# Optimization experiments

Hardware: AMD Instinct MI355X
Metric: run time of the kernel (lower is better)

Reference implementation:

```python
import jax, jax.numpy as jnp
import numpy as np

LN_EPS = 1e-3   # keras LayerNormalization default epsilon
STAB = 1e-3     # performer relu-kernel numerical stabilizer
N = 2           # number of blocks per branch


def layer_norm(x, g, b):
    m = jnp.mean(x, axis=-1, keepdims=True)
    v = jnp.mean(jnp.square(x - m), axis=-1, keepdims=True)
    return (x - m) * jax.lax.rsqrt(v + LN_EPS) * g + b


def favor(q_in, kv_in, Wq, Wk, Wv, Wo):
    # Performer FAVOR attention, relu kernel features (google-research fast_attention,
    # projection_matrix_type=None). q/k/v head projections have no bias.
    q = jnp.einsum('bld,dhm->blhm', q_in, Wq)
    k = jnp.einsum('bsd,dhm->bshm', kv_in, Wk)
    v = jnp.einsum('bsd,dhm->bshm', kv_in, Wv)
    norm = q.shape[-1] ** -0.25  # 1/sqrt(sqrt(head_dim))
    qp = jax.nn.relu(q * norm) + STAB
    kp = jax.nn.relu(k * norm) + STAB
    kv = jnp.einsum('bshm,bshd->bhmd', kp, v)
    num = jnp.einsum('blhm,bhmd->blhd', qp, kv)
    den = jnp.einsum('blhm,bhm->blh', qp, kp.sum(axis=1))
    out = num / den[..., None]
    return jnp.einsum('blhd,hde->ble', out, Wo)


def forward(obj_inputs, road_inputs,
            rg_dense_W, rg_dense_b, rg_qkv_W, rg_qkv_b,
            rg_Wq, rg_Wk, rg_Wv, rg_Wo, rg_ln_g, rg_ln_b, rg_fc_W, rg_fc_b,
            rg_out_W, rg_out_b,
            dense_W, dense_b, pos_emb,
            Wq, Wk, Wv, Wo, ln_g, ln_b, fc_W, fc_b):
    rgH = rg_dense_W.shape[1]
    # ---- roadgraph branch: performer self-attention blocks ----
    x = jax.nn.relu(road_inputs @ rg_dense_W + rg_dense_b)
    for i in range(N):
        qkv = jax.nn.relu(x @ rg_qkv_W + rg_qkv_b)
        q = qkv[..., :rgH]  # k,v splits unused by FastSelfAttention (it re-projects q)
        attn = favor(q, q, rg_Wq[i], rg_Wk[i], rg_Wv[i], rg_Wo[i])
        n = layer_norm(attn + x, rg_ln_g[i], rg_ln_b[i])
        y = jax.nn.relu(n @ rg_fc_W[i] + rg_fc_b[i])
        x = layer_norm(n + y, rg_ln_g[i], rg_ln_b[i])  # original reuses ln_block_1
    rg_out = jax.nn.relu(x @ rg_out_W + rg_out_b)
    # ---- object branch: performer cross-attention blocks ----
    x = jax.nn.relu(obj_inputs @ dense_W + dense_b)
    x = x + pos_emb  # learned position embedding, [T, H]
    for i in range(N):
        attn = favor(x, rg_out, Wq[i], Wk[i], Wv[i], Wo[i])
        n = layer_norm(attn + x, ln_g[i], ln_b[i])
        y = jax.nn.relu(n @ fc_W[i] + fc_b[i])
        x = layer_norm(n + y, ln_g[i], ln_b[i])  # original reuses ln_block_1
    return x


def setup_inputs() -> dict:
    B, T, V = 8, 128, 512
    S, F = 8192, 8
    rgH, H = 16, 1024
    rh, rd = 4, 4     # rg heads, head_dim
    h, d = 16, 64     # cross heads, head_dim
    keys = iter(jax.random.split(jax.random.key(0), 64))
    def rnd(shape, scale=1.0):
        return jax.random.normal(next(keys), shape, dtype=jnp.float32) * scale
    return {
        'obj_inputs': rnd((B, T, V)),
        'road_inputs': rnd((B, S, F)),
        'rg_dense_W': rnd((F, rgH), F ** -0.5), 'rg_dense_b': jnp.zeros((rgH,), jnp.float32),
        'rg_qkv_W': rnd((rgH, 3 * rgH), rgH ** -0.5), 'rg_qkv_b': jnp.zeros((3 * rgH,), jnp.float32),
        'rg_Wq': rnd((N, rgH, rh, rd), rgH ** -0.5),
        'rg_Wk': rnd((N, rgH, rh, rd), rgH ** -0.5),
        'rg_Wv': rnd((N, rgH, rh, rd), rgH ** -0.5),
        'rg_Wo': rnd((N, rh, rd, rgH), rgH ** -0.5),
        'rg_ln_g': jnp.ones((N, rgH), jnp.float32), 'rg_ln_b': jnp.zeros((N, rgH), jnp.float32),
        'rg_fc_W': rnd((N, rgH, rgH), rgH ** -0.5), 'rg_fc_b': jnp.zeros((N, rgH), jnp.float32),
        'rg_out_W': rnd((rgH, H), rgH ** -0.5), 'rg_out_b': jnp.zeros((H,), jnp.float32),
        'dense_W': rnd((V, H), V ** -0.5), 'dense_b': jnp.zeros((H,), jnp.float32),
        'pos_emb': rnd((T, H), 0.02),
        'Wq': rnd((N, H, h, d), H ** -0.5),
        'Wk': rnd((N, H, h, d), H ** -0.5),
        'Wv': rnd((N, H, h, d), H ** -0.5),
        'Wo': rnd((N, h, d, H), H ** -0.5),
        'ln_g': jnp.ones((N, H), jnp.float32), 'ln_b': jnp.zeros((N, H), jnp.float32),
        'fc_W': rnd((N, H, H), H ** -0.5), 'fc_b': jnp.zeros((N, H), jnp.float32),
    }


def reference(obj_inputs, road_inputs, rg_dense_W, rg_dense_b, rg_qkv_W, rg_qkv_b,
              rg_Wq, rg_Wk, rg_Wv, rg_Wo, rg_ln_g, rg_ln_b, rg_fc_W, rg_fc_b,
              rg_out_W, rg_out_b, dense_W, dense_b, pos_emb,
              Wq, Wk, Wv, Wo, ln_g, ln_b, fc_W, fc_b):
    return forward(obj_inputs, road_inputs, rg_dense_W, rg_dense_b, rg_qkv_W, rg_qkv_b,
                   rg_Wq, rg_Wk, rg_Wv, rg_Wo, rg_ln_g, rg_ln_b, rg_fc_W, rg_fc_b,
                   rg_out_W, rg_out_b, dense_W, dense_b, pos_emb,
                   Wq, Wk, Wv, Wo, ln_g, ln_b, fc_W, fc_b)
```

## Files before the change

kernel.cpp:

```cpp
#include <hip/hip_runtime.h>

typedef unsigned short u16;
typedef unsigned int u32;

using s8v = __attribute__((ext_vector_type(8))) short;
using f4v = __attribute__((ext_vector_type(4))) float;

#define LN_EPS 0.001f
#define STAB 0.001f
#define NORM_OBJ 0.35355339059327373f
#define NORM_ROAD 0.7071067811865476f

__device__ __forceinline__ float bf2f(u16 v) { return __uint_as_float(((u32)v) << 16); }
__device__ __forceinline__ u16 f2bf(float f) {
  u32 u = __float_as_uint(f);
  u32 r = (u + 0x7fffu + ((u >> 16) & 1u)) >> 16;
  return (u16)r;
}
__device__ __forceinline__ f4v mfma16(s8v a, s8v b, f4v c) {
  return __builtin_amdgcn_mfma_f32_16x16x32_bf16(a, b, c, 0, 0, 0);
}
__device__ __forceinline__ void ldsload16(void* lds, const void* g) {
  __builtin_amdgcn_global_load_lds((const __attribute__((address_space(1))) u32*)g,
                                   (__attribute__((address_space(3))) u32*)lds, 16, 0, 0);
}

struct TPair { const float* s; u16* d; };
struct TP11 { TPair p[11]; };

__global__ __launch_bounds__(256) void transpose_kernel(TP11 ps, int K, int N) {
  const float* __restrict__ src = ps.p[blockIdx.z].s;
  u16* __restrict__ dst = ps.p[blockIdx.z].d;
  int n0 = blockIdx.x * 64, k0 = blockIdx.y * 64;
  int t = threadIdx.x;
  __shared__ __align__(16) u16 lt[64 * 72];
#pragma unroll
  for (int j = 0; j < 4; ++j) {
    int p = t + 256 * j;
    int r = p >> 4, cb = p & 15;
    float4 v = *(const float4*)(src + (size_t)(k0 + r) * N + n0 + cb * 4);
    lt[r * 72 + cb * 4 + 0] = f2bf(v.x);
    lt[r * 72 + cb * 4 + 1] = f2bf(v.y);
    lt[r * 72 + cb * 4 + 2] = f2bf(v.z);
    lt[r * 72 + cb * 4 + 3] = f2bf(v.w);
  }
  __syncthreads();
#pragma unroll
  for (int j = 0; j < 2; ++j) {
    int q = t + 256 * j;
    int on = q >> 3, ocb = q & 7;
    u16 e[8];
#pragma unroll
    for (int i = 0; i < 8; ++i) e[i] = lt[(ocb * 8 + i) * 72 + on];
    uint4 v;
    v.x = (u32)e[0] | ((u32)e[1] << 16);
    v.y = (u32)e[2] | ((u32)e[3] << 16);
    v.z = (u32)e[4] | ((u32)e[5] << 16);
    v.w = (u32)e[6] | ((u32)e[7] << 16);
    *(uint4*)(dst + (size_t)(n0 + on) * K + k0 + ocb * 8) = v;
  }
}

__global__ __launch_bounds__(256) void cvt_kernel(const float* __restrict__ src,
                                                  u16* __restrict__ dst) {
  int i = (blockIdx.x * 256 + threadIdx.x) * 4;
  float4 v = *(const float4*)(src + i);
  uint2 o;
  o.x = (u32)f2bf(v.x) | ((u32)f2bf(v.y) << 16);
  o.y = (u32)f2bf(v.z) | ((u32)f2bf(v.w) << 16);
  *(uint2*)(dst + i) = o;
}

__global__ __launch_bounds__(256) void r0_kernel(const float* __restrict__ road,
    const float* __restrict__ W, const float* __restrict__ bias, float* __restrict__ x) {
  int row = blockIdx.x * 256 + threadIdx.x;
  float in[8];
  float4 v0 = *(const float4*)(road + (size_t)row * 8);
  float4 v1 = *(const float4*)(road + (size_t)row * 8 + 4);
  in[0] = v0.x; in[1] = v0.y; in[2] = v0.z; in[3] = v0.w;
  in[4] = v1.x; in[5] = v1.y; in[6] = v1.z; in[7] = v1.w;
#pragma unroll
  for (int j = 0; j < 16; ++j) {
    float s = bias[j];
#pragma unroll
    for (int c = 0; c < 8; ++c) s += in[c] * W[c * 16 + j];
    x[(size_t)row * 16 + j] = fmaxf(s, 0.f);
  }
}

__global__ __launch_bounds__(256) void ra_kernel(const float* __restrict__ x,
    const float* __restrict__ qkvW, const float* __restrict__ qkvb,
    const float* __restrict__ Wk, const float* __restrict__ Wv,
    float* __restrict__ kvr, float* __restrict__ ksr) {
  int t = threadIdx.x;
  int row = blockIdx.x * 256 + t;
  int b = row >> 13;
  float xv[16];
#pragma unroll
  for (int e = 0; e < 16; ++e) xv[e] = x[(size_t)row * 16 + e];
  float q16[16];
#pragma unroll
  for (int j = 0; j < 16; ++j) {
    float s = qkvb[j];
#pragma unroll
    for (int c = 0; c < 16; ++c) s += xv[c] * qkvW[c * 48 + j];
    q16[j] = fmaxf(s, 0.f);
  }
  float kp[16], vh[16];
#pragma unroll
  for (int hm = 0; hm < 16; ++hm) {
    float sk = 0.f, sv = 0.f;
#pragma unroll
    for (int c = 0; c < 16; ++c) {
      float q = q16[c];
      sk += q * Wk[c * 16 + hm];
      sv += q * Wv[c * 16 + hm];
    }
    kp[hm] = fmaxf(sk * NORM_ROAD, 0.f) + STAB;
    vh[hm] = sv;
  }
  __shared__ float l[80];
  if (t < 80) l[t] = 0.f;
  __syncthreads();
#pragma unroll
  for (int h = 0; h < 4; ++h)
#pragma unroll
    for (int m = 0; m < 4; ++m) {
      float kpv = kp[h * 4 + m];
      atomicAdd(&l[64 + h * 4 + m], kpv);
#pragma unroll
      for (int d = 0; d < 4; ++d) atomicAdd(&l[h * 16 + m * 4 + d], kpv * vh[h * 4 + d]);
    }
  __syncthreads();
  if (t < 64) atomicAdd(&kvr[b * 64 + t], l[t]);
  else if (t < 80) atomicAdd(&ksr[b * 16 + (t - 64)], l[t]);
}

__device__ __forceinline__ void ln16(const float* tv, const float* g, const float* bb, float* o) {
  float m = 0.f;
#pragma unroll
  for (int e = 0; e < 16; ++e) m += tv[e];
  m *= (1.f / 16.f);
  float var = 0.f;
#pragma unroll
  for (int e = 0; e < 16; ++e) { float d = tv[e] - m; var += d * d; }
  var *= (1.f / 16.f);
  float rstd = rsqrtf(var + LN_EPS);
#pragma unroll
  for (int e = 0; e < 16; ++e) o[e] = (tv[e] - m) * rstd * g[e] + bb[e];
}

__global__ __launch_bounds__(256) void rb_kernel(float* __restrict__ x,
    const float* __restrict__ qkvW, const float* __restrict__ qkvb,
    const float* __restrict__ Wq, const float* __restrict__ Wo,
    const float* __restrict__ lng, const float* __restrict__ lnb,
    const float* __restrict__ fcW, const float* __restrict__ fcb,
    const float* __restrict__ kvr, const float* __restrict__ ksr) {
  int row = blockIdx.x * 256 + threadIdx.x;
  int b = row >> 13;
  float xv[16];
#pragma unroll
  for (int e = 0; e < 16; ++e) xv[e] = x[(size_t)row * 16 + e];
  float q16[16];
#pragma unroll
  for (int j = 0; j < 16; ++j) {
    float s = qkvb[j];
#pragma unroll
    for (int c = 0; c < 16; ++c) s += xv[c] * qkvW[c * 48 + j];
    q16[j] = fmaxf(s, 0.f);
  }
  float qp[16];
#pragma unroll
  for (int hm = 0; hm < 16; ++hm) {
    float s = 0.f;
#pragma unroll
    for (int c = 0; c < 16; ++c) s += q16[c] * Wq[c * 16 + hm];
    qp[hm] = fmaxf(s * NORM_ROAD, 0.f) + STAB;
  }
  float attn[16];
#pragma unroll
  for (int e = 0; e < 16; ++e) attn[e] = 0.f;
#pragma unroll
  for (int h = 0; h < 4; ++h) {
    float den = 0.f;
#pragma unroll
    for (int m = 0; m < 4; ++m) den += qp[h * 4 + m] * ksr[b * 16 + h * 4 + m];
    float od[4];
#pragma unroll
    for (int d = 0; d < 4; ++d) {
      float num = 0.f;
#pragma unroll
      for (int m = 0; m < 4; ++m) num += qp[h * 4 + m] * kvr[b * 64 + h * 16 + m * 4 + d];
      od[d] = num / den;
    }
#pragma unroll
    for (int d = 0; d < 4; ++d)
#pragma unroll
      for (int e = 0; e < 16; ++e) attn[e] += od[d] * Wo[(h * 4 + d) * 16 + e];
  }
  float tv[16], n[16], o2[16];
#pragma unroll
  for (int e = 0; e < 16; ++e) tv[e] = attn[e] + xv[e];
  ln16(tv, lng, lnb, n);
#pragma unroll
  for (int j = 0; j < 16; ++j) {
    float s = fcb[j];
#pragma unroll
    for (int e = 0; e < 16; ++e) s += n[e] * fcW[e * 16 + j];
    tv[j] = n[j] + fmaxf(s, 0.f);
  }
  ln16(tv, lng, lnb, o2);
#pragma unroll
  for (int e = 0; e < 16; ++e) x[(size_t)row * 16 + e] = o2[e];
}

__global__ __launch_bounds__(256) void rc_kernel(const float* __restrict__ x,
    const float* __restrict__ W, const float* __restrict__ bias, u16* __restrict__ out) {
  const int t = threadIdx.x;
  const int cg = t & 63, rg = t >> 6;
  const int c0 = blockIdx.x * 256 + cg * 4;
  const int r0 = blockIdx.y * 16;
  __shared__ float lx[256];
  lx[t] = x[(size_t)(r0 + (t >> 4)) * 16 + (t & 15)];
  __syncthreads();
  float4 wv[16];
#pragma unroll
  for (int c = 0; c < 16; ++c) wv[c] = *(const float4*)(W + (size_t)c * 1024 + c0);
  float4 bv = *(const float4*)(bias + c0);
#pragma unroll
  for (int k = 0; k < 4; ++k) {
    int rr = rg * 4 + k;
    float s0 = bv.x, s1 = bv.y, s2 = bv.z, s3 = bv.w;
#pragma unroll
    for (int c = 0; c < 16; ++c) {
      float xv = lx[rr * 16 + c];
      s0 += xv * wv[c].x; s1 += xv * wv[c].y; s2 += xv * wv[c].z; s3 += xv * wv[c].w;
    }
    uint2 o;
    o.x = (u32)f2bf(fmaxf(s0, 0.f)) | ((u32)f2bf(fmaxf(s1, 0.f)) << 16);
    o.y = (u32)f2bf(fmaxf(s2, 0.f)) | ((u32)f2bf(fmaxf(s3, 0.f)) << 16);
    *(uint2*)(out + (size_t)(r0 + rr) * 1024 + c0) = o;
  }
}

__global__ __launch_bounds__(256) void gemm_kernel(
    const u16* __restrict__ A, const u16* __restrict__ BT, int K,
    float* __restrict__ outF, u16* __restrict__ outB,
    const float* __restrict__ bias, const float* __restrict__ resF, int resmod,
    float scale, int do_relu, float post) {
  const int n0 = blockIdx.x * 128, m0 = blockIdx.y * 128;
  const int t = threadIdx.x;
  const int wid = t >> 6, lane = t & 63, quad = lane >> 4, m16 = lane & 15;
  const int wm = wid >> 1, wn = wid & 1;
  const int lrr = lane >> 3;
  const int lcs = (((lane & 7) ^ lrr) * 8);
  const int sw = m16 & 7;
  __shared__ __align__(16) u16 smem[2 * 128 * 64];
  u16* Al = smem;
  u16* Bl = smem + 128 * 64;
  f4v acc[4][4];
#pragma unroll
  for (int i = 0; i < 4; ++i)
#pragma unroll
    for (int j = 0; j < 4; ++j) acc[i][j] = {0.f, 0.f, 0.f, 0.f};

  for (int kc = 0; kc < K; kc += 64) {
    __syncthreads();
#pragma unroll
    for (int j = 0; j < 4; ++j) {
      int rbase = wid * 32 + j * 8;
      ldsload16(Al + rbase * 64, A + (size_t)(m0 + rbase + lrr) * K + kc + lcs);
      ldsload16(Bl + rbase * 64, BT + (size_t)(n0 + rbase + lrr) * K + kc + lcs);
    }
    __syncthreads();
#pragma unroll
    for (int ko = 0; ko < 64; ko += 32) {
      int g0 = ko >> 3;
      s8v af[4], bfr[4];
#pragma unroll
      for (int tm = 0; tm < 4; ++tm)
        af[tm] = *(const s8v*)(Al + (wm * 64 + tm * 16 + m16) * 64 + ((g0 + quad) ^ sw) * 8);
#pragma unroll
      for (int tn = 0; tn < 4; ++tn)
        bfr[tn] = *(const s8v*)(Bl + (wn * 64 + tn * 16 + m16) * 64 + ((g0 + quad) ^ sw) * 8);
#pragma unroll
      for (int tm = 0; tm < 4; ++tm)
#pragma unroll
        for (int tn = 0; tn < 4; ++tn)
          acc[tm][tn] = mfma16(af[tm], bfr[tn], acc[tm][tn]);
    }
  }
#pragma unroll
  for (int tm = 0; tm < 4; ++tm)
#pragma unroll
    for (int tn = 0; tn < 4; ++tn)
#pragma unroll
      for (int r = 0; r < 4; ++r) {
        int row = m0 + wm * 64 + tm * 16 + quad * 4 + r;
        int col = n0 + wn * 64 + tn * 16 + m16;
        float v = acc[tm][tn][r] * scale;
        if (bias) v += bias[col];
        if (do_relu) v = fmaxf(v, 0.f);
        v += post;
        if (resF) v += resF[(size_t)(row % resmod) * 1024 + col];
        if (outF) outF[(size_t)row * 1024 + col] = v;
        if (outB) outB[(size_t)row * 1024 + col] = f2bf(v);
      }
}

__global__ __launch_bounds__(512) void kv_kernel(
    const u16* __restrict__ rgout,
    const u16* __restrict__ WkT0, const u16* __restrict__ WvT0,
    const u16* __restrict__ WkT1, const u16* __restrict__ WvT1,
    float* __restrict__ kv, float* __restrict__ ksum) {
  const int mt = blockIdx.x, y = blockIdx.y, b = blockIdx.z;
  const int lay = y >> 3, hp = y & 7;
  const u16* __restrict__ WkT = lay ? WkT1 : WkT0;
  const u16* __restrict__ WvT = lay ? WvT1 : WvT0;
  kv += (size_t)lay * 524288;
  ksum += (size_t)lay * 8192;
  const int t = threadIdx.x;
  const int wid = t >> 6, lane = t & 63, quad = lane >> 4, m16 = lane & 15;
  const int wm = wid >> 2, wn = wid & 3;
  const int lrr = lane >> 3;
  const int lcs = (((lane & 7) ^ lrr) * 8);
  const int sw = m16 & 7;
  const int HSZ = 64 * 136;
  __shared__ __align__(16) u16 smem[4 * 64 * 136];
  u16* Al = smem;
  u16* Bl = smem + 128 * 64;
  const size_t abase = ((size_t)b * 8192 + (size_t)mt * 128) * 1024;
  f4v acc[4][4];
#pragma unroll
  for (int i = 0; i < 4; ++i)
#pragma unroll
    for (int j = 0; j < 4; ++j) acc[i][j] = {0.f, 0.f, 0.f, 0.f};

  for (int kc = 0; kc < 1024; kc += 64) {
    __syncthreads();
#pragma unroll
    for (int j = 0; j < 2; ++j) {
      int rbase = wid * 16 + j * 8;
      ldsload16(Al + rbase * 64, rgout + abase + (size_t)(rbase + lrr) * 1024 + kc + lcs);
    }
#pragma unroll
    for (int j = 0; j < 4; ++j) {
      int rbase = wid * 32 + j * 8;
      int r = rbase + lrr;
      int h = hp * 2 + (r >> 7), rr = r & 127;
      const u16* bsrc = (rr < 64) ? (WkT + (size_t)(h * 64 + rr) * 1024)
                                  : (WvT + (size_t)(h * 64 + (rr - 64)) * 1024);
      ldsload16(Bl + rbase * 64, bsrc + kc + lcs);
    }
    __syncthreads();
#pragma unroll
    for (int ko = 0; ko < 64; ko += 32) {
      int g0 = ko >> 3;
      s8v af[4], bfr[4];
#pragma unroll
      for (int tm = 0; tm < 4; ++tm)
        af[tm] = *(const s8v*)(Al + (wm * 64 + tm * 16 + m16) * 64 + ((g0 + quad) ^ sw) * 8);
#pragma unroll
      for (int tn = 0; tn < 4; ++tn)
        bfr[tn] = *(const s8v*)(Bl + (wn * 64 + tn * 16 + m16) * 64 + ((g0 + quad) ^ sw) * 8);
#pragma unroll
      for (int tm = 0; tm < 4; ++tm)
#pragma unroll
        for (int tn = 0; tn < 4; ++tn)
          acc[tm][tn] = mfma16(af[tm], bfr[tn], acc[tm][tn]);
    }
  }
  __syncthreads();
  {
    int hh = wn >> 1;
    u16* dst = smem + (size_t)(hh * 2 + (wn & 1)) * HSZ;
    const int iskp = (wn & 1) == 0;
    const int sbase = wm * 64 + quad * 4;
#pragma unroll
    for (int tm = 0; tm < 4; ++tm)
#pragma unroll
      for (int tn = 0; tn < 4; ++tn) {
        float v0 = acc[tm][tn][0], v1 = acc[tm][tn][1];
        float v2 = acc[tm][tn][2], v3 = acc[tm][tn][3];
        if (iskp) {
          v0 = fmaxf(v0 * NORM_OBJ, 0.f) + STAB;
          v1 = fmaxf(v1 * NORM_OBJ, 0.f) + STAB;
          v2 = fmaxf(v2 * NORM_OBJ, 0.f) + STAB;
          v3 = fmaxf(v3 * NORM_OBJ, 0.f) + STAB;
        }
        uint2 o;
        o.x = (u32)f2bf(v0) | ((u32)f2bf(v1) << 16);
        o.y = (u32)f2bf(v2) | ((u32)f2bf(v3) << 16);
        int feat = tn * 16 + m16;
        *(uint2*)(dst + feat * 136 + sbase + tm * 16) = o;
      }
  }
  __syncthreads();
  if (t < 128) {
    int hh = t >> 6, m = t & 63;
    const u16* base = smem + (size_t)(hh * 2) * HSZ + m * 136;
    float s = 0.f;
#pragma unroll
    for (int i = 0; i < 128; i += 8) {
      uint4 v = *(const uint4*)(base + i);
      u32 a[4] = {v.x, v.y, v.z, v.w};
#pragma unroll
      for (int q = 0; q < 4; ++q) {
        s += __uint_as_float(a[q] << 16);
        s += __uint_as_float(a[q] & 0xffff0000u);
      }
    }
    atomicAdd(&ksum[(size_t)(b * 16 + hp * 2 + hh) * 64 + m], s);
  }
  {
    int hh = wid >> 2, mq = wid & 3;
    const u16* KPh = smem + (size_t)(hh * 2) * HSZ;
    const u16* Vh = KPh + HSZ;
    f4v a2[4];
#pragma unroll
    for (int tn = 0; tn < 4; ++tn) a2[tn] = {0.f, 0.f, 0.f, 0.f};
#pragma unroll
    for (int ks = 0; ks < 128; ks += 32) {
      s8v af = *(const s8v*)(KPh + (mq * 16 + m16) * 136 + ks + quad * 8);
#pragma unroll
      for (int tn = 0; tn < 4; ++tn) {
        s8v bv = *(const s8v*)(Vh + (tn * 16 + m16) * 136 + ks + quad * 8);
        a2[tn] = mfma16(af, bv, a2[tn]);
      }
    }
    int h = hp * 2 + hh;
#pragma unroll
    for (int tn = 0; tn < 4; ++tn)
#pragma unroll
      for (int r = 0; r < 4; ++r) {
        int m = mq * 16 + quad * 4 + r;
        int d = tn * 16 + m16;
        atomicAdd(&kv[((size_t)(b * 16 + h) * 64 + m) * 64 + d], a2[tn][r]);
      }
  }
}

__global__ __launch_bounds__(256) void q2_kernel(const u16* __restrict__ qp,
    const float* __restrict__ kv, const float* __restrict__ ks, u16* __restrict__ out) {
  int wid = threadIdx.x >> 6, lane = threadIdx.x & 63;
  int row = blockIdx.x * 4 + wid;
  int b = row >> 7;
  int h0 = blockIdx.y * 4;
  for (int h = h0; h < h0 + 4; ++h) {
    const float* kvp = kv + (size_t)((b * 16 + h) * 64) * 64;
    const float* ksp = ks + (size_t)(b * 16 + h) * 64;
    const u16* qpp = qp + (size_t)row * 1024 + h * 64;
    float num = 0.f, den = 0.f;
    for (int m = 0; m < 64; ++m) {
      float qv = bf2f(qpp[m]);
      num += qv * kvp[m * 64 + lane];
      den += qv * ksp[m];
    }
    out[(size_t)row * 1024 + h * 64 + lane] = f2bf(num / den);
  }
}

__global__ __launch_bounds__(256) void ln_kernel(const float* __restrict__ in,
    const float* __restrict__ g, const float* __restrict__ bb,
    float* __restrict__ outF, u16* __restrict__ outB) {
  int row = blockIdx.x, t = threadIdx.x;
  const float* x = in + (size_t)row * 1024;
  float v[4];
  float s = 0.f, ss = 0.f;
#pragma unroll
  for (int j = 0; j < 4; ++j) {
    v[j] = x[t + 256 * j];
    s += v[j];
    ss += v[j] * v[j];
  }
  __shared__ float rs[256], rss[256];
  rs[t] = s; rss[t] = ss;
  __syncthreads();
  for (int o = 128; o > 0; o >>= 1) {
    if (t < o) { rs[t] += rs[t + o]; rss[t] += rss[t + o]; }
    __syncthreads();
  }
  float mean = rs[0] * (1.f / 1024.f);
  float var = rss[0] * (1.f / 1024.f) - mean * mean;
  float rstd = rsqrtf(var + LN_EPS);
#pragma unroll
  for (int j = 0; j < 4; ++j) {
    int c = t + 256 * j;
    float o = (v[j] - mean) * rstd * g[c] + bb[c];
    if (outF) outF[(size_t)row * 1024 + c] = o;
    if (outB) outB[(size_t)row * 1024 + c] = f2bf(o);
  }
}

static constexpr size_t MBy = 1048576;
static constexpr size_t OFF_XROAD = 0;
static constexpr size_t OFF_RGOUT = 4 * MBy;
static constexpr size_t OFF_KVR = OFF_RGOUT + 128 * MBy;
static constexpr size_t OFF_KSR = OFF_KVR + 2048;
static constexpr size_t OFF_KVO = OFF_KVR + 4096;
static constexpr size_t OFF_KSO = OFF_KVO + 4 * MBy;
static constexpr size_t OFF_WT = OFF_KSO + 65536;
static constexpr size_t OFF_XOBJ = OFF_WT + 21 * MBy;
static constexpr size_t OFF_XOBJB = OFF_XOBJ + 4 * MBy;
static constexpr size_t OFF_QP = OFF_XOBJB + 2 * MBy;
static constexpr size_t OFF_FOUT = OFF_QP + 2 * MBy;
static constexpr size_t OFF_T1 = OFF_FOUT + 2 * MBy;
static constexpr size_t OFF_N = OFF_T1 + 4 * MBy;
static constexpr size_t OFF_NB = OFF_N + 4 * MBy;
static constexpr size_t OFF_OBJB = OFF_NB + 2 * MBy;

extern "C" void kernel_launch(void* const* d_in, const int* in_sizes, int n_in,
                              void* d_out, int out_size, void* d_ws, size_t ws_size,
                              hipStream_t stream) {
  (void)in_sizes; (void)n_in; (void)out_size; (void)ws_size;
  const float* obj = (const float*)d_in[0];
  const float* road = (const float*)d_in[1];
  const float* rgdW = (const float*)d_in[2];
  const float* rgdb = (const float*)d_in[3];
  const float* qkvW = (const float*)d_in[4];
  const float* qkvb = (const float*)d_in[5];
  const float* rgWq = (const float*)d_in[6];
  const float* rgWk = (const float*)d_in[7];
  const float* rgWv = (const float*)d_in[8];
  const float* rgWo = (const float*)d_in[9];
  const float* rglng = (const float*)d_in[10];
  const float* rglnb = (const float*)d_in[11];
  const float* rgfcW = (const float*)d_in[12];
  const float* rgfcb = (const float*)d_in[13];
  const float* rgoW = (const float*)d_in[14];
  const float* rgob = (const float*)d_in[15];
  const float* denW = (const float*)d_in[16];
  const float* denb = (const float*)d_in[17];
  const float* pose = (const float*)d_in[18];
  const float* Wq = (const float*)d_in[19];
  const float* Wk = (const float*)d_in[20];
  const float* Wv = (const float*)d_in[21];
  const float* Wo = (const float*)d_in[22];
  const float* lng = (const float*)d_in[23];
  const float* lnb = (const float*)d_in[24];
  const float* fcW = (const float*)d_in[25];
  const float* fcb = (const float*)d_in[26];

  char* w = (char*)d_ws;
  float* xroad = (float*)(w + OFF_XROAD);
  u16* rgout = (u16*)(w + OFF_RGOUT);
  float* kvr = (float*)(w + OFF_KVR);
  float* ksr = (float*)(w + OFF_KSR);
  float* kvo = (float*)(w + OFF_KVO);
  float* kso = (float*)(w + OFF_KSO);
  u16* wt = (u16*)(w + OFF_WT);
  float* xobj = (float*)(w + OFF_XOBJ);
  u16* xobjb = (u16*)(w + OFF_XOBJB);
  u16* qpB = (u16*)(w + OFF_QP);
  u16* fout = (u16*)(w + OFF_FOUT);
  float* t1 = (float*)(w + OFF_T1);
  float* nF = (float*)(w + OFF_N);
  u16* nB = (u16*)(w + OFF_NB);
  u16* objb = (u16*)(w + OFF_OBJB);

  const size_t E = 1048576;
  u16* wqT[2] = {wt + 0 * E, wt + 1 * E};
  u16* wkT[2] = {wt + 2 * E, wt + 3 * E};
  u16* wvT[2] = {wt + 4 * E, wt + 5 * E};
  u16* woT[2] = {wt + 6 * E, wt + 7 * E};
  u16* fcT[2] = {wt + 8 * E, wt + 9 * E};
  u16* denT = wt + 10 * E;

  TP11 tb;
  const float* srcs[10] = {Wq, Wq + E, Wk, Wk + E, Wv, Wv + E, Wo, Wo + E, fcW, fcW + E};
  u16* dsts[10] = {wqT[0], wqT[1], wkT[0], wkT[1], wvT[0], wvT[1], woT[0], woT[1], fcT[0], fcT[1]};
  for (int j = 0; j < 11; ++j) { tb.p[j].s = srcs[j < 10 ? j : 0]; tb.p[j].d = dsts[j < 10 ? j : 0]; }
  transpose_kernel<<<dim3(16, 16, 10), 256, 0, stream>>>(tb, 1024, 1024);
  TP11 td;
  for (int j = 0; j < 11; ++j) { td.p[j].s = denW; td.p[j].d = denT; }
  transpose_kernel<<<dim3(16, 8, 1), 256, 0, stream>>>(td, 512, 1024);
  cvt_kernel<<<dim3(512), 256, 0, stream>>>(obj, objb);

  r0_kernel<<<dim3(256), 256, 0, stream>>>(road, rgdW, rgdb, xroad);
  for (int i = 0; i < 2; ++i) {
    hipMemsetAsync(w + OFF_KVR, 0, 2560, stream);
    ra_kernel<<<dim3(256), 256, 0, stream>>>(xroad, qkvW, qkvb, rgWk + i * 256, rgWv + i * 256,
                                             kvr, ksr);
    rb_kernel<<<dim3(256), 256, 0, stream>>>(xroad, qkvW, qkvb, rgWq + i * 256, rgWo + i * 256,
                                             rglng + i * 16, rglnb + i * 16, rgfcW + i * 256,
                                             rgfcb + i * 16, kvr, ksr);
  }
  rc_kernel<<<dim3(4, 4096), 256, 0, stream>>>(xroad, rgoW, rgob, rgout);

  hipMemsetAsync(w + OFF_KVO, 0, 4 * MBy + 65536, stream);
  kv_kernel<<<dim3(64, 16, 8), 512, 0, stream>>>(rgout, wkT[0], wvT[0], wkT[1], wvT[1], kvo, kso);

  gemm_kernel<<<dim3(8, 8), 256, 0, stream>>>(objb, denT, 512, xobj, xobjb, denb, pose, 128,
                                              1.f, 1, 0.f);

  for (int i = 0; i < 2; ++i) {
    gemm_kernel<<<dim3(8, 8), 256, 0, stream>>>(xobjb, wqT[i], 1024, nullptr, qpB, nullptr,
                                                nullptr, 1024, NORM_OBJ, 1, STAB);
    q2_kernel<<<dim3(256, 4), 256, 0, stream>>>(qpB, kvo + (size_t)i * 524288,
                                                kso + (size_t)i * 8192, fout);
    gemm_kernel<<<dim3(8, 8), 256, 0, stream>>>(fout, woT[i], 1024, t1, nullptr, nullptr, xobj,
                                                1024, 1.f, 0, 0.f);
    ln_kernel<<<dim3(1024), 256, 0, stream>>>(t1, lng + i * 1024, lnb + i * 1024, nF, nB);
    gemm_kernel<<<dim3(8, 8), 256, 0, stream>>>(nB, fcT[i], 1024, t1, nullptr, fcb + i * 1024, nF,
                                                1024, 1.f, 1, 0.f);
    if (i == 0)
      ln_kernel<<<dim3(1024), 256, 0, stream>>>(t1, lng, lnb, xobj, xobjb);
    else
      ln_kernel<<<dim3(1024), 256, 0, stream>>>(t1, lng + 1024, lnb + 1024, (float*)d_out, nullptr);
  }
}
```

Baseline: 1.484 ms.

## Split-K object GEMMs, fuse epilogues into consumers, and merge road kernels

The 1024x1024x1024 object-branch GEMMs, which previously launched only 64 blocks, now use a split-K of 2. Each half writes fp32 partials, and the consumers sum them: q2 applies the relu feature map, and the LN kernel applies bias, relu and the residual. The roadgraph kernels are fused so the next block's kv accumulation runs inside the previous block's kernel. This removes a memset and several launches, and the two transposes are merged into one launch. The cost is extra fp32 partial traffic through global memory.

```diff
diff --git a/kernel.cpp b/kernel.cpp
--- a/kernel.cpp
+++ b/kernel.cpp
@@ -25,20 +25,23 @@
                                    (__attribute__((address_space(3))) u32*)lds, 16, 0, 0);
 }
 
-struct TPair { const float* s; u16* d; };
+struct TPair { const float* s; u16* d; int K; };
 struct TP11 { TPair p[11]; };
 
-__global__ __launch_bounds__(256) void transpose_kernel(TP11 ps, int K, int N) {
-  const float* __restrict__ src = ps.p[blockIdx.z].s;
-  u16* __restrict__ dst = ps.p[blockIdx.z].d;
+__global__ __launch_bounds__(256) void transpose_kernel(TP11 ps) {
+  const TPair pp = ps.p[blockIdx.z];
+  const int K = pp.K;
+  const float* __restrict__ src = pp.s;
+  u16* __restrict__ dst = pp.d;
   int n0 = blockIdx.x * 64, k0 = blockIdx.y * 64;
+  if (k0 >= K) return;
   int t = threadIdx.x;
   __shared__ __align__(16) u16 lt[64 * 72];
 #pragma unroll
   for (int j = 0; j < 4; ++j) {
     int p = t + 256 * j;
     int r = p >> 4, cb = p & 15;
-    float4 v = *(const float4*)(src + (size_t)(k0 + r) * N + n0 + cb * 4);
+    float4 v = *(const float4*)(src + (size_t)(k0 + r) * 1024 + n0 + cb * 4);
     lt[r * 72 + cb * 4 + 0] = f2bf(v.x);
     lt[r * 72 + cb * 4 + 1] = f2bf(v.y);
     lt[r * 72 + cb * 4 + 2] = f2bf(v.z);
@@ -71,33 +74,60 @@
   *(uint2*)(dst + i) = o;
 }
 
-__global__ __launch_bounds__(256) void r0_kernel(const float* __restrict__ road,
-    const float* __restrict__ W, const float* __restrict__ bias, float* __restrict__ x) {
-  int row = blockIdx.x * 256 + threadIdx.x;
-  float in[8];
-  float4 v0 = *(const float4*)(road + (size_t)row * 8);
-  float4 v1 = *(const float4*)(road + (size_t)row * 8 + 4);
-  in[0] = v0.x; in[1] = v0.y; in[2] = v0.z; in[3] = v0.w;
-  in[4] = v1.x; in[5] = v1.y; in[6] = v1.z; in[7] = v1.w;
-#pragma unroll
-  for (int j = 0; j < 16; ++j) {
-    float s = bias[j];
-#pragma unroll
-    for (int c = 0; c < 8; ++c) s += in[c] * W[c * 16 + j];
-    x[(size_t)row * 16 + j] = fmaxf(s, 0.f);
-  }
-}
-
-__global__ __launch_bounds__(256) void ra_kernel(const float* __restrict__ x,
+__device__ __forceinline__ void road_acc(const float* q16, const float* Wk, const float* Wv,
+                                         float* l, int t, int b,
+                                         float* kvr, float* ksr) {
+  float kp[16], vh[16];
+#pragma unroll
+  for (int hm = 0; hm < 16; ++hm) {
+    float sk = 0.f, sv = 0.f;
+#pragma unroll
+    for (int c = 0; c < 16; ++c) {
+      float q = q16[c];
+      sk += q * Wk[c * 16 + hm];
+      sv += q * Wv[c * 16 + hm];
+    }
+    kp[hm] = fmaxf(sk * NORM_ROAD, 0.f) + STAB;
+    vh[hm] = sv;
+  }
+  if (t < 80) l[t] = 0.f;
+  __syncthreads();
+#pragma unroll
+  for (int h = 0; h < 4; ++h)
+#pragma unroll
+    for (int m = 0; m < 4; ++m) {
+      float kpv = kp[h * 4 + m];
+      atomicAdd(&l[64 + h * 4 + m], kpv);
+#pragma unroll
+      for (int d = 0; d < 4; ++d) atomicAdd(&l[h * 16 + m * 4 + d], kpv * vh[h * 4 + d]);
+    }
+  __syncthreads();
+  if (t < 64) atomicAdd(&kvr[b * 64 + t], l[t]);
+  else if (t < 80) atomicAdd(&ksr[b * 16 + (t - 64)], l[t]);
+}
+
+__global__ __launch_bounds__(256) void r0ra_kernel(const float* __restrict__ road,
+    const float* __restrict__ W, const float* __restrict__ bias, float* __restrict__ x,
     const float* __restrict__ qkvW, const float* __restrict__ qkvb,
     const float* __restrict__ Wk, const float* __restrict__ Wv,
     float* __restrict__ kvr, float* __restrict__ ksr) {
   int t = threadIdx.x;
   int row = blockIdx.x * 256 + t;
   int b = row >> 13;
+  float in[8];
+  float4 v0 = *(const float4*)(road + (size_t)row * 8);
+  float4 v1 = *(const float4*)(road + (size_t)row * 8 + 4);
+  in[0] = v0.x; in[1] = v0.y; in[2] = v0.z; in[3] = v0.w;
+  in[4] = v1.x; in[5] = v1.y; in[6] = v1.z; in[7] = v1.w;
   float xv[16];
 #pragma unroll
-  for (int e = 0; e < 16; ++e) xv[e] = x[(size_t)row * 16 + e];
+  for (int j = 0; j < 16; ++j) {
+    float s = bias[j];
+#pragma unroll
+    for (int c = 0; c < 8; ++c) s += in[c] * W[c * 16 + j];
+    xv[j] = fmaxf(s, 0.f);
+    x[(size_t)row * 16 + j] = xv[j];
+  }
   float q16[16];
 #pragma unroll
   for (int j = 0; j < 16; ++j) {
@@ -106,34 +136,8 @@
     for (int c = 0; c < 16; ++c) s += xv[c] * qkvW[c * 48 + j];
     q16[j] = fmaxf(s, 0.f);
   }
-  float kp[16], vh[16];
-#pragma unroll
-  for (int hm = 0; hm < 16; ++hm) {
-    float sk = 0.f, sv = 0.f;
-#pragma unroll
-    for (int c = 0; c < 16; ++c) {
-      float q = q16[c];
-      sk += q * Wk[c * 16 + hm];
-      sv += q * Wv[c * 16 + hm];
-    }
-    kp[hm] = fmaxf(sk * NORM_ROAD, 0.f) + STAB;
-    vh[hm] = sv;
-  }
   __shared__ float l[80];
-  if (t < 80) l[t] = 0.f;
-  __syncthreads();
-#pragma unroll
-  for (int h = 0; h < 4; ++h)
-#pragma unroll
-    for (int m = 0; m < 4; ++m) {
-      float kpv = kp[h * 4 + m];
-      atomicAdd(&l[64 + h * 4 + m], kpv);
-#pragma unroll
-      for (int d = 0; d < 4; ++d) atomicAdd(&l[h * 16 + m * 4 + d], kpv * vh[h * 4 + d]);
-    }
-  __syncthreads();
-  if (t < 64) atomicAdd(&kvr[b * 64 + t], l[t]);
-  else if (t < 80) atomicAdd(&ksr[b * 16 + (t - 64)], l[t]);
+  road_acc(q16, Wk, Wv, l, t, b, kvr, ksr);
 }
 
 __device__ __forceinline__ void ln16(const float* tv, const float* g, const float* bb, float* o) {
@@ -150,13 +154,16 @@
   for (int e = 0; e < 16; ++e) o[e] = (tv[e] - m) * rstd * g[e] + bb[e];
 }
 
-__global__ __launch_bounds__(256) void rb_kernel(float* __restrict__ x,
+__global__ __launch_bounds__(256) void rbra_kernel(float* __restrict__ x,
     const float* __restrict__ qkvW, const float* __restrict__ qkvb,
     const float* __restrict__ Wq, const float* __restrict__ Wo,
     const float* __restrict__ lng, const float* __restrict__ lnb,
     const float* __restrict__ fcW, const float* __restrict__ fcb,
-    const float* __restrict__ kvr, const float* __restrict__ ksr) {
-  int row = blockIdx.x * 256 + threadIdx.x;
+    const float* __restrict__ kvr, const float* __restrict__ ksr,
+    const float* __restrict__ Wkn, const float* __restrict__ Wvn,
+    float* __restrict__ kvrn, float* __restrict__ ksrn, int do_next) {
+  int t = threadIdx.x;
+  int row = blockIdx.x * 256 + t;
   int b = row >> 13;
   float xv[16];
 #pragma unroll
@@ -212,6 +219,18 @@
   ln16(tv, lng, lnb, o2);
 #pragma unroll
   for (int e = 0; e < 16; ++e) x[(size_t)row * 16 + e] = o2[e];
+  __shared__ float l[80];
+  if (do_next) {
+    float q16n[16];
+#pragma unroll
+    for (int j = 0; j < 16; ++j) {
+      float s = qkvb[j];
+#pragma unroll
+      for (int c = 0; c < 16; ++c) s += o2[c] * qkvW[c * 48 + j];
+      q16n[j] = fmaxf(s, 0.f);
+    }
+    road_acc(q16n, Wkn, Wvn, l, t, b, kvrn, ksrn);
+  }
 }
 
 __global__ __launch_bounds__(256) void rc_kernel(const float* __restrict__ x,
@@ -247,7 +266,7 @@
     const u16* __restrict__ A, const u16* __restrict__ BT, int K,
     float* __restrict__ outF, u16* __restrict__ outB,
     const float* __restrict__ bias, const float* __restrict__ resF, int resmod,
-    float scale, int do_relu, float post) {
+    float scale, int do_relu, float post, size_t zstride) {
   const int n0 = blockIdx.x * 128, m0 = blockIdx.y * 128;
   const int t = threadIdx.x;
   const int wid = t >> 6, lane = t & 63, quad = lane >> 4, m16 = lane & 15;
@@ -255,6 +274,9 @@
   const int lrr = lane >> 3;
   const int lcs = (((lane & 7) ^ lrr) * 8);
   const int sw = m16 & 7;
+  if (outF) outF += (size_t)blockIdx.z * zstride;
+  const int kper = K / gridDim.z;
+  const int kbeg = blockIdx.z * kper;
   __shared__ __align__(16) u16 smem[2 * 128 * 64];
   u16* Al = smem;
   u16* Bl = smem + 128 * 64;
@@ -264,7 +286,7 @@
 #pragma unroll
     for (int j = 0; j < 4; ++j) acc[i][j] = {0.f, 0.f, 0.f, 0.f};
 
-  for (int kc = 0; kc < K; kc += 64) {
+  for (int kc = kbeg; kc < kbeg + kper; kc += 64) {
     __syncthreads();
 #pragma unroll
     for (int j = 0; j < 4; ++j) {
@@ -440,7 +462,8 @@
   }
 }
 
-__global__ __launch_bounds__(256) void q2_kernel(const u16* __restrict__ qp,
+__global__ __launch_bounds__(256) void q2_kernel(const float* __restrict__ p0,
+    const float* __restrict__ p1,
     const float* __restrict__ kv, const float* __restrict__ ks, u16* __restrict__ out) {
   int wid = threadIdx.x >> 6, lane = threadIdx.x & 63;
   int row = blockIdx.x * 4 + wid;
@@ -449,29 +472,36 @@
   for (int h = h0; h < h0 + 4; ++h) {
     const float* kvp = kv + (size_t)((b * 16 + h) * 64) * 64;
     const float* ksp = ks + (size_t)(b * 16 + h) * 64;
-    const u16* qpp = qp + (size_t)row * 1024 + h * 64;
+    size_t base = (size_t)row * 1024 + h * 64;
     float num = 0.f, den = 0.f;
     for (int m = 0; m < 64; ++m) {
-      float qv = bf2f(qpp[m]);
+      float qv = fmaxf((p0[base + m] + p1[base + m]) * NORM_OBJ, 0.f) + STAB;
       num += qv * kvp[m * 64 + lane];
       den += qv * ksp[m];
     }
-    out[(size_t)row * 1024 + h * 64 + lane] = f2bf(num / den);
-  }
-}
-
-__global__ __launch_bounds__(256) void ln_kernel(const float* __restrict__ in,
+    out[base + lane] = f2bf(num / den);
+  }
+}
+
+__global__ __launch_bounds__(256) void ln_kernel(const float* __restrict__ p0,
+    const float* __restrict__ p1, const float* __restrict__ bias,
+    const float* __restrict__ res, int do_relu,
     const float* __restrict__ g, const float* __restrict__ bb,
     float* __restrict__ outF, u16* __restrict__ outB) {
   int row = blockIdx.x, t = threadIdx.x;
-  const float* x = in + (size_t)row * 1024;
+  size_t base = (size_t)row * 1024;
   float v[4];
   float s = 0.f, ss = 0.f;
 #pragma unroll
   for (int j = 0; j < 4; ++j) {
-    v[j] = x[t + 256 * j];
-    s += v[j];
-    ss += v[j] * v[j];
+    int c = t + 256 * j;
+    float x = p0[base + c] + p1[base + c];
+    if (bias) x += bias[c];
+    if (do_relu) x = fmaxf(x, 0.f);
+    if (res) x += res[base + c];
+    v[j] = x;
+    s += x;
+    ss += x * x;
   }
   __shared__ float rs[256], rss[256];
   rs[t] = s; rss[t] = ss;
@@ -487,8 +517,8 @@
   for (int j = 0; j < 4; ++j) {
     int c = t + 256 * j;
     float o = (v[j] - mean) * rstd * g[c] + bb[c];
-    if (outF) outF[(size_t)row * 1024 + c] = o;
-    if (outB) outB[(size_t)row * 1024 + c] = f2bf(o);
+    if (outF) outF[base + c] = o;
+    if (outB) outB[base + c] = f2bf(o);
   }
 }
 
@@ -496,16 +526,15 @@
 static constexpr size_t OFF_XROAD = 0;
 static constexpr size_t OFF_RGOUT = 4 * MBy;
 static constexpr size_t OFF_KVR = OFF_RGOUT + 128 * MBy;
-static constexpr size_t OFF_KSR = OFF_KVR + 2048;
-static constexpr size_t OFF_KVO = OFF_KVR + 4096;
+static constexpr size_t OFF_KSR = OFF_KVR + 4096;
+static constexpr size_t OFF_KVO = OFF_KVR + 8192;
 static constexpr size_t OFF_KSO = OFF_KVO + 4 * MBy;
 static constexpr size_t OFF_WT = OFF_KSO + 65536;
 static constexpr size_t OFF_XOBJ = OFF_WT + 21 * MBy;
 static constexpr size_t OFF_XOBJB = OFF_XOBJ + 4 * MBy;
-static constexpr size_t OFF_QP = OFF_XOBJB + 2 * MBy;
-static constexpr size_t OFF_FOUT = OFF_QP + 2 * MBy;
-static constexpr size_t OFF_T1 = OFF_FOUT + 2 * MBy;
-static constexpr size_t OFF_N = OFF_T1 + 4 * MBy;
+static constexpr size_t OFF_P0 = OFF_XOBJB + 2 * MBy;
+static constexpr size_t OFF_FOUT = OFF_P0 + 8 * MBy;
+static constexpr size_t OFF_N = OFF_FOUT + 2 * MBy;
 static constexpr size_t OFF_NB = OFF_N + 4 * MBy;
 static constexpr size_t OFF_OBJB = OFF_NB + 2 * MBy;
 
@@ -551,9 +580,9 @@
   u16* wt = (u16*)(w + OFF_WT);
   float* xobj = (float*)(w + OFF_XOBJ);
   u16* xobjb = (u16*)(w + OFF_XOBJB);
-  u16* qpB = (u16*)(w + OFF_QP);
+  float* P0 = (float*)(w + OFF_P0);
+  float* P1 = P0 + 1048576;
   u16* fout = (u16*)(w + OFF_FOUT);
-  float* t1 = (float*)(w + OFF_T1);
   float* nF = (float*)(w + OFF_N);
   u16* nB = (u16*)(w + OFF_NB);
   u16* objb = (u16*)(w + OFF_OBJB);
@@ -567,45 +596,46 @@
   u16* denT = wt + 10 * E;
 
   TP11 tb;
-  const float* srcs[10] = {Wq, Wq + E, Wk, Wk + E, Wv, Wv + E, Wo, Wo + E, fcW, fcW + E};
-  u16* dsts[10] = {wqT[0], wqT[1], wkT[0], wkT[1], wvT[0], wvT[1], woT[0], woT[1], fcT[0], fcT[1]};
-  for (int j = 0; j < 11; ++j) { tb.p[j].s = srcs[j < 10 ? j : 0]; tb.p[j].d = dsts[j < 10 ? j : 0]; }
-  transpose_kernel<<<dim3(16, 16, 10), 256, 0, stream>>>(tb, 1024, 1024);
-  TP11 td;
-  for (int j = 0; j < 11; ++j) { td.p[j].s = denW; td.p[j].d = denT; }
-  transpose_kernel<<<dim3(16, 8, 1), 256, 0, stream>>>(td, 512, 1024);
+  const float* srcs[11] = {Wq, Wq + E, Wk, Wk + E, Wv, Wv + E, Wo, Wo + E, fcW, fcW + E, denW};
+  u16* dsts[11] = {wqT[0], wqT[1], wkT[0], wkT[1], wvT[0], wvT[1], woT[0], woT[1],
+                   fcT[0], fcT[1], denT};
+  for (int j = 0; j < 11; ++j) { tb.p[j].s = srcs[j]; tb.p[j].d = dsts[j]; tb.p[j].K = (j == 10) ? 512 : 1024; }
+  transpose_kernel<<<dim3(16, 16, 11), 256, 0, stream>>>(tb);
   cvt_kernel<<<dim3(512), 256, 0, stream>>>(obj, objb);
 
-  r0_kernel<<<dim3(256), 256, 0, stream>>>(road, rgdW, rgdb, xroad);
-  for (int i = 0; i < 2; ++i) {
-    hipMemsetAsync(w + OFF_KVR, 0, 2560, stream);
-    ra_kernel<<<dim3(256), 256, 0, stream>>>(xroad, qkvW, qkvb, rgWk + i * 256, rgWv + i * 256,
-                                             kvr, ksr);
-    rb_kernel<<<dim3(256), 256, 0, stream>>>(xroad, qkvW, qkvb, rgWq + i * 256, rgWo + i * 256,
-                                             rglng + i * 16, rglnb + i * 16, rgfcW + i * 256,
-                                             rgfcb + i * 16, kvr, ksr);
-  }
+  hipMemsetAsync(w + OFF_KVR, 0, 5120, stream);
+  r0ra_kernel<<<dim3(256), 256, 0, stream>>>(road, rgdW, rgdb, xroad, qkvW, qkvb,
+                                             rgWk, rgWv, kvr, ksr);
+  rbra_kernel<<<dim3(256), 256, 0, stream>>>(xroad, qkvW, qkvb, rgWq, rgWo, rglng, rglnb,
+                                             rgfcW, rgfcb, kvr, ksr,
+                                             rgWk + 256, rgWv + 256, kvr + 512, ksr + 128, 1);
+  rbra_kernel<<<dim3(256), 256, 0, stream>>>(xroad, qkvW, qkvb, rgWq + 256, rgWo + 256,
+                                             rglng + 16, rglnb + 16, rgfcW + 256, rgfcb + 16,
+                                             kvr + 512, ksr + 128,
+                                             nullptr, nullptr, nullptr, nullptr, 0);
   rc_kernel<<<dim3(4, 4096), 256, 0, stream>>>(xroad, rgoW, rgob, rgout);
 
   hipMemsetAsync(w + OFF_KVO, 0, 4 * MBy + 65536, stream);
   kv_kernel<<<dim3(64, 16, 8), 512, 0, stream>>>(rgout, wkT[0], wvT[0], wkT[1], wvT[1], kvo, kso);
 
-  gemm_kernel<<<dim3(8, 8), 256, 0, stream>>>(objb, denT, 512, xobj, xobjb, denb, pose, 128,
-                                              1.f, 1, 0.f);
+  gemm_kernel<<<dim3(8, 8, 1), 256, 0, stream>>>(objb, denT, 512, xobj, xobjb, denb, pose, 128,
+                                                 1.f, 1, 0.f, 0);
 
   for (int i = 0; i < 2; ++i) {
-    gemm_kernel<<<dim3(8, 8), 256, 0, stream>>>(xobjb, wqT[i], 1024, nullptr, qpB, nullptr,
-                                                nullptr, 1024, NORM_OBJ, 1, STAB);
-    q2_kernel<<<dim3(256, 4), 256, 0, stream>>>(qpB, kvo + (size_t)i * 524288,
+    gemm_kernel<<<dim3(8, 8, 2), 256, 0, stream>>>(xobjb, wqT[i], 1024, P0, nullptr, nullptr,
+                                                   nullptr, 1024, 1.f, 0, 0.f, 1048576);
+    q2_kernel<<<dim3(256, 4), 256, 0, stream>>>(P0, P1, kvo + (size_t)i * 524288,
                                                 kso + (size_t)i * 8192, fout);
-    gemm_kernel<<<dim3(8, 8), 256, 0, stream>>>(fout, woT[i], 1024, t1, nullptr, nullptr, xobj,
-                                                1024, 1.f, 0, 0.f);
-    ln_kernel<<<dim3(1024), 256, 0, stream>>>(t1, lng + i * 1024, lnb + i * 1024, nF, nB);
-    gemm_kernel<<<dim3(8, 8), 256, 0, stream>>>(nB, fcT[i], 1024, t1, nullptr, fcb + i * 1024, nF,
-                                                1024, 1.f, 1, 0.f);
+    gemm_kernel<<<dim3(8, 8, 2), 256, 0, stream>>>(fout, woT[i], 1024, P0, nullptr, nullptr,
+                                                   nullptr, 1024, 1.f, 0, 0.f, 1048576);
+    ln_kernel<<<dim3(1024), 256, 0, stream>>>(P0, P1, nullptr, xobj, 0,
+                                              lng + i * 1024, lnb + i * 1024, nF, nB);
+    gemm_kernel<<<dim3(8, 8, 2), 256, 0, stream>>>(nB, fcT[i], 1024, P0, nullptr, nullptr,
+                                                   nullptr, 1024, 1.f, 0, 0.f, 1048576);
     if (i == 0)
-      ln_kernel<<<dim3(1024), 256, 0, stream>>>(t1, lng, lnb, xobj, xobjb);
+      ln_kernel<<<dim3(1024), 256, 0, stream>>>(P0, P1, fcb, nF, 1, lng, lnb, xobj, xobjb);
     else
-      ln_kernel<<<dim3(1024), 256, 0, stream>>>(t1, lng + 1024, lnb + 1024, (float*)d_out, nullptr);
-  }
-}
+      ln_kernel<<<dim3(1024), 256, 0, stream>>>(P0, P1, fcb + 1024, nF, 1, lng + 1024,
+                                                lnb + 1024, (float*)d_out, nullptr);
+  }
+}
```

Measured after the change: 1.380 ms. 1.08x faster.
